# Kernel optimization log

Hardware: AMD Instinct MI355X
Metric: run time of the kernel (lower is better)

Reference implementation:

```python
import jax, jax.numpy as jnp
import numpy as np

D_MODEL = 1024
NUM_HEADS = 16
D_HEAD = D_MODEL // NUM_HEADS
B, T_Q, T_K = 2, 2048, 2048


def setup_inputs() -> dict:
    key = jax.random.key(0)
    ks = jax.random.split(key, 7)
    s = 0.02
    return {
        "query": jax.random.normal(ks[0], (B, T_Q, D_MODEL), jnp.float32),
        "key_value": jax.random.normal(ks[1], (B, T_K, D_MODEL), jnp.float32),
        "mask": jax.random.randint(ks[2], (B, 1, T_Q, T_K), 0, 2, jnp.int32),
        "rel_pos_bias": jax.random.normal(ks[3], (NUM_HEADS, T_Q, T_K), jnp.float32),
        "Wq": jax.random.normal(ks[4], (D_MODEL, D_MODEL), jnp.float32) * s,
        "Wkv": jax.random.normal(ks[5], (D_MODEL, 2 * D_MODEL), jnp.float32) * s,
        "Wo": jax.random.normal(ks[6], (D_MODEL, D_MODEL), jnp.float32) * s,
    }


def reference(query, key_value, mask, rel_pos_bias, Wq, Wkv, Wo):
    Bq, Tq, D = query.shape
    Tk = key_value.shape[1]
    H, Dh = NUM_HEADS, D_HEAD
    q = (query @ Wq).reshape(Bq, Tq, H, Dh)              # [B,Tq,H,Dh]
    kv = (key_value @ Wkv).reshape(Bq, Tk, 2, H, Dh)
    k, v = kv[:, :, 0], kv[:, :, 1]                      # [B,Tk,H,Dh]
    scale = 1.0 / jnp.sqrt(jnp.asarray(Dh, q.dtype))
    scores = jnp.einsum("bqhd,bkhd->bhqk", q, k) * scale  # [B,H,Tq,Tk]
    scores = scores + rel_pos_bias[None]                  # bias broadcast over batch
    scores = jnp.where(mask == 0, -jnp.inf, scores)
    attn = jax.nn.softmax(scores, axis=-1)
    out = jnp.einsum("bhqk,bkhd->bqhd", attn, v).reshape(Bq, Tq, D)
    return out @ Wo
```

## Files before the change

### kernel.cpp

```cpp
#include <hip/hip_runtime.h>

typedef unsigned short u16;
typedef unsigned long long u64;
typedef __attribute__((ext_vector_type(4))) float f32x4;
typedef __attribute__((ext_vector_type(4))) unsigned short u16x4;
typedef __attribute__((ext_vector_type(8))) short short8;

#define GLOAD16(G, L) __builtin_amdgcn_global_load_lds( \
    (const __attribute__((address_space(1))) void*)(G), \
    (__attribute__((address_space(3))) void*)(L), 16, 0, 0)

__device__ __forceinline__ u16 f2bf(float f) {
  union { float f; unsigned u; } c; c.f = f;
  unsigned u = c.u;
  u += 0x7FFFu + ((u >> 16) & 1u);
  return (u16)(u >> 16);
}

__device__ __forceinline__ void store_out(u16* p, float v) { *p = f2bf(v); }
__device__ __forceinline__ void store_out(float* p, float v) { *p = v; }

__global__ void k_cvt(const float* __restrict__ in, u16* __restrict__ out, int n4) {
  int i = blockIdx.x * blockDim.x + threadIdx.x;
  if (i >= n4) return;
  const f32x4 v = *(const f32x4*)(in + (size_t)i * 4);
  u16x4 o;
  o[0] = f2bf(v[0]); o[1] = f2bf(v[1]); o[2] = f2bf(v[2]); o[3] = f2bf(v[3]);
  *(u16x4*)(out + (size_t)i * 4) = o;
}

__global__ void k_tcvt(const float* __restrict__ src, u16* __restrict__ dst,
                       int R, int C, float scale) {
  __shared__ float t[32][33];
  int bx = blockIdx.x * 32;
  int by = blockIdx.y * 32;
  int tx = threadIdx.x, ty = threadIdx.y;
  #pragma unroll
  for (int j = 0; j < 32; j += 8)
    t[ty + j][tx] = src[(size_t)(by + ty + j) * C + bx + tx];
  __syncthreads();
  #pragma unroll
  for (int j = 0; j < 32; j += 8)
    dst[(size_t)(bx + ty + j) * R + by + tx] = f2bf(t[tx][ty + j] * scale);
}

__global__ void k_tv(const u16* __restrict__ kv, u16* __restrict__ vt) {
  __shared__ u16 t[32][34];
  int b = blockIdx.z;
  int tb = blockIdx.x * 32;
  int db = blockIdx.y * 32;
  int tx = threadIdx.x, ty = threadIdx.y;
  #pragma unroll
  for (int j = 0; j < 32; j += 8)
    t[ty + j][tx] = kv[(size_t)(b * 2048 + tb + ty + j) * 2048 + 1024 + db + tx];
  __syncthreads();
  #pragma unroll
  for (int j = 0; j < 32; j += 8)
    vt[(size_t)(b * 1024 + db + ty + j) * 2048 + tb + tx] = t[tx][ty + j];
}

__global__ void k_pm(const int* __restrict__ mask, unsigned* __restrict__ bits, int nw) {
  int w = blockIdx.x * blockDim.x + threadIdx.x;
  if (w >= nw) return;
  const int4* p = (const int4*)(mask + (size_t)w * 32);
  unsigned b = 0;
  #pragma unroll
  for (int j = 0; j < 8; ++j) {
    int4 v = p[j];
    b |= (v.x != 0 ? 1u : 0u) << (j * 4);
    b |= (v.y != 0 ? 1u : 0u) << (j * 4 + 1);
    b |= (v.z != 0 ? 1u : 0u) << (j * 4 + 2);
    b |= (v.w != 0 ? 1u : 0u) << (j * 4 + 3);
  }
  bits[w] = b;
}

template <typename OUT_T>
__global__ __launch_bounds__(256) void k_gemm(
    const u16* __restrict__ A, const u16* __restrict__ Bt,
    OUT_T* __restrict__ C, int M, int N, int K)
{
  __shared__ u16 As[128 * 64];
  __shared__ u16 Bs[128 * 64];
  const int tid = threadIdx.x;
  const int lane = tid & 63;
  const int w = tid >> 6;
  const int wr = w >> 1, wc = w & 1;
  const int l16 = lane & 15, lh = lane >> 4;
  const size_t tm = blockIdx.x, tn = blockIdx.y;

  f32x4 acc[4][4] = {};

  for (int kt = 0; kt < K; kt += 64) {
    #pragma unroll
    for (int i = 0; i < 4; ++i) {
      int flat = i * 256 + tid;
      int row = flat >> 3, cb = flat & 7;
      GLOAD16(A + (tm * 128 + row) * K + kt + ((cb ^ (row & 7)) * 8),
              (char*)As + flat * 16);
    }
    #pragma unroll
    for (int i = 0; i < 4; ++i) {
      int flat = i * 256 + tid;
      int row = flat >> 3, cb = flat & 7;
      GLOAD16(Bt + (tn * 128 + row) * K + kt + ((cb ^ (row & 7)) * 8),
              (char*)Bs + flat * 16);
    }
    __syncthreads();
    #pragma unroll
    for (int kk = 0; kk < 2; ++kk) {
      short8 a[4], b[4];
      #pragma unroll
      for (int mi = 0; mi < 4; ++mi) {
        int row = wr * 64 + mi * 16 + l16;
        a[mi] = *(const short8*)&As[row * 64 + ((kk * 32 + lh * 8) ^ ((row & 7) * 8))];
      }
      #pragma unroll
      for (int ni = 0; ni < 4; ++ni) {
        int row = wc * 64 + ni * 16 + l16;
        b[ni] = *(const short8*)&Bs[row * 64 + ((kk * 32 + lh * 8) ^ ((row & 7) * 8))];
      }
      #pragma unroll
      for (int mi = 0; mi < 4; ++mi)
        #pragma unroll
        for (int ni = 0; ni < 4; ++ni)
          acc[mi][ni] = __builtin_amdgcn_mfma_f32_16x16x32_bf16(a[mi], b[ni], acc[mi][ni], 0, 0, 0);
    }
    __syncthreads();
  }
  #pragma unroll
  for (int mi = 0; mi < 4; ++mi)
    #pragma unroll
    for (int ni = 0; ni < 4; ++ni)
      #pragma unroll
      for (int r = 0; r < 4; ++r) {
        size_t row = tm * 128 + wr * 64 + mi * 16 + lh * 4 + r;
        size_t col = tn * 128 + wc * 64 + ni * 16 + l16;
        store_out(&C[row * N + col], acc[mi][ni][r]);
      }
}

__global__ __launch_bounds__(512, 4) void k_attn(
    const u16* __restrict__ Qp,
    const u16* __restrict__ KVp,
    const u16* __restrict__ Vt,
    const float* __restrict__ bias,
    const unsigned* __restrict__ mbits,
    u16* __restrict__ Ob)
{
  __shared__ u16 Ks[2 * 2 * 64 * 64];
  __shared__ u16 Vs[2 * 2 * 64 * 64];
  __shared__ u16 Ps[8 * 16 * 64];
  const int tid = threadIdx.x;
  const int lane = tid & 63;
  const int w = tid >> 6;
  const int bw = w >> 2;
  const int qs = (w & 3) * 16;
  const int qt = blockIdx.x;
  const int h  = blockIdx.y;
  const int l16 = lane & 15, lh = lane >> 4;

  const int srow = tid >> 3, scb = tid & 7;
  const int scol = (scb ^ (srow & 7)) * 8;
  const u16* ksrc0 = KVp + ((size_t)(          srow)) * 2048 + h * 64 + scol;
  const u16* kstep = KVp;
  const u16* vsrc0 = Vt  + ((size_t)(h * 64 + srow)) * 2048 + scol;

  short8 qf[2];
  {
    size_t row = (size_t)bw * 2048 + qt * 64 + qs + l16;
    qf[0] = *(const short8*)&Qp[row * 1024 + h * 64 + lh * 8];
    qf[1] = *(const short8*)&Qp[row * 1024 + h * 64 + 32 + lh * 8];
  }

  const size_t bias_row = ((size_t)h * 2048 + qt * 64 + qs + lh * 4) * 2048;
  const size_t mrow0 = ((size_t)bw * 2048 + qt * 64 + qs + lh * 4) * 64;

  f32x4 oacc[4] = {};
  float lpart[4] = {0.f, 0.f, 0.f, 0.f};

  {
    GLOAD16(ksrc0 + (size_t)(0 * 2048) * 2048, &Ks[0 * 8192 + 0 * 4096 + tid * 8]);
    GLOAD16(ksrc0 + (size_t)(1 * 2048) * 2048, &Ks[0 * 8192 + 1 * 4096 + tid * 8]);
    GLOAD16(vsrc0 + (size_t)(0 * 1024) * 2048, &Vs[0 * 8192 + 0 * 4096 + tid * 8]);
    GLOAD16(vsrc0 + (size_t)(1 * 1024) * 2048, &Vs[0 * 8192 + 1 * 4096 + tid * 8]);
  }
  f32x4 bias_cur[4];
  u64 mw_cur[4];
  #pragma unroll
  for (int ni = 0; ni < 4; ++ni)
    #pragma unroll
    for (int r = 0; r < 4; ++r)
      bias_cur[ni][r] = bias[bias_row + (size_t)r * 2048 + ni * 16 + l16];
  #pragma unroll
  for (int r = 0; r < 4; ++r)
    mw_cur[r] = *(const u64*)&mbits[mrow0 + (size_t)r * 64];

  asm volatile("s_waitcnt vmcnt(0)" ::: "memory");
  __builtin_amdgcn_s_barrier();

  for (int kt = 0; kt < 32; ++kt) {
    const int cur = kt & 1;

    f32x4 bias_nxt[4];
    u64 mw_nxt[4];
    if (kt + 1 < 32) {
      const int nb = cur ^ 1;
      const size_t kro = (size_t)((kt + 1) * 64) * 2048;
      const size_t vco = (size_t)((kt + 1) * 64);
      GLOAD16(ksrc0 + (size_t)(0 * 2048) * 2048 + kro, &Ks[nb * 8192 + 0 * 4096 + tid * 8]);
      GLOAD16(ksrc0 + (size_t)(1 * 2048) * 2048 + kro, &Ks[nb * 8192 + 1 * 4096 + tid * 8]);
      GLOAD16(vsrc0 + (size_t)(0 * 1024) * 2048 + vco, &Vs[nb * 8192 + 0 * 4096 + tid * 8]);
      GLOAD16(vsrc0 + (size_t)(1 * 1024) * 2048 + vco, &Vs[nb * 8192 + 1 * 4096 + tid * 8]);
      #pragma unroll
      for (int ni = 0; ni < 4; ++ni)
        #pragma unroll
        for (int r = 0; r < 4; ++r)
          bias_nxt[ni][r] = bias[bias_row + (size_t)r * 2048 + (kt + 1) * 64 + ni * 16 + l16];
      #pragma unroll
      for (int r = 0; r < 4; ++r)
        mw_nxt[r] = *(const u64*)&mbits[mrow0 + (size_t)r * 64 + (kt + 1) * 2];
    }

    f32x4 s[4];
    #pragma unroll
    for (int ni = 0; ni < 4; ++ni) s[ni] = bias_cur[ni];
    #pragma unroll
    for (int kk = 0; kk < 2; ++kk) {
      short8 kf[4];
      #pragma unroll
      for (int ni = 0; ni < 4; ++ni) {
        int row = ni * 16 + l16;
        kf[ni] = *(const short8*)&Ks[cur * 8192 + bw * 4096 + row * 64 + ((kk * 32 + lh * 8) ^ ((row & 7) * 8))];
      }
      #pragma unroll
      for (int ni = 0; ni < 4; ++ni)
        s[ni] = __builtin_amdgcn_mfma_f32_16x16x32_bf16(qf[kk], kf[ni], s[ni], 0, 0, 0);
    }

    #pragma unroll
    for (int r = 0; r < 4; ++r) {
      unsigned w0 = (unsigned)mw_cur[r], w1 = (unsigned)(mw_cur[r] >> 32);
      int row16 = lh * 4 + r;
      #pragma unroll
      for (int ni = 0; ni < 4; ++ni) {
        unsigned word = (ni & 2) ? w1 : w0;
        unsigned bit = (word >> ((ni & 1) * 16 + l16)) & 1u;
        float p = bit ? __expf(s[ni][r]) : 0.f;
        lpart[r] += p;
        int col = ni * 16 + l16;
        Ps[w * 1024 + row16 * 64 + (col ^ ((row16 & 7) * 8))] = f2bf(p);
      }
    }

    #pragma unroll
    for (int kk = 0; kk < 2; ++kk) {
      short8 pa, vf[4];
      {
        int row = l16;
        pa = *(const short8*)&Ps[w * 1024 + row * 64 + ((kk * 32 + lh * 8) ^ ((row & 7) * 8))];
      }
      #pragma unroll
      for (int di = 0; di < 4; ++di) {
        int row = di * 16 + l16;
        vf[di] = *(const short8*)&Vs[cur * 8192 + bw * 4096 + row * 64 + ((kk * 32 + lh * 8) ^ ((row & 7) * 8))];
      }
      #pragma unroll
      for (int di = 0; di < 4; ++di)
        oacc[di] = __builtin_amdgcn_mfma_f32_16x16x32_bf16(pa, vf[di], oacc[di], 0, 0, 0);
    }

    #pragma unroll
    for (int ni = 0; ni < 4; ++ni) bias_cur[ni] = bias_nxt[ni];
    #pragma unroll
    for (int r = 0; r < 4; ++r) mw_cur[r] = mw_nxt[r];

    asm volatile("s_waitcnt vmcnt(0)" ::: "memory");
    __builtin_amdgcn_s_barrier();
  }

  #pragma unroll
  for (int r = 0; r < 4; ++r) {
    float sum = lpart[r];
    sum += __shfl_xor(sum, 1);
    sum += __shfl_xor(sum, 2);
    sum += __shfl_xor(sum, 4);
    sum += __shfl_xor(sum, 8);
    float inv = 1.0f / sum;
    size_t row = (size_t)bw * 2048 + qt * 64 + qs + lh * 4 + r;
    #pragma unroll
    for (int di = 0; di < 4; ++di)
      Ob[row * 1024 + h * 64 + di * 16 + l16] = f2bf(oacc[di][r] * inv);
  }
}

extern "C" void kernel_launch(void* const* d_in, const int* in_sizes, int n_in,
                              void* d_out, int out_size, void* d_ws, size_t ws_size,
                              hipStream_t stream) {
  const float* query     = (const float*)d_in[0];
  const float* key_value = (const float*)d_in[1];
  const int*   mask      = (const int*)d_in[2];
  const float* bias      = (const float*)d_in[3];
  const float* Wq        = (const float*)d_in[4];
  const float* Wkv       = (const float*)d_in[5];
  const float* Wo        = (const float*)d_in[6];
  float* out = (float*)d_out;

  char* ws = (char*)d_ws;
  u16* qb   = (u16*)(ws);
  u16* kvb  = (u16*)(ws + 8388608);
  u16* WqT  = (u16*)(ws + 16777216);
  u16* WkvT = (u16*)(ws + 18874368);
  u16* WoT  = (u16*)(ws + 23068672);
  u16* Qp   = (u16*)(ws + 25165824);
  u16* KVp  = (u16*)(ws + 33554432);
  u16* Vt   = (u16*)(ws + 50331648);
  u16* Ob   = (u16*)(ws + 58720256);
  unsigned* mb = (unsigned*)(ws + 67108864);

  dim3 tb(32, 8);
  k_cvt<<<4096, 256, 0, stream>>>(query, qb, 1048576);
  k_cvt<<<4096, 256, 0, stream>>>(key_value, kvb, 1048576);
  k_tcvt<<<dim3(32, 32), tb, 0, stream>>>(Wq,  WqT,  1024, 1024, 0.125f);
  k_tcvt<<<dim3(64, 32), tb, 0, stream>>>(Wkv, WkvT, 1024, 2048, 1.0f);
  k_tcvt<<<dim3(32, 32), tb, 0, stream>>>(Wo,  WoT,  1024, 1024, 1.0f);
  k_pm<<<1024, 256, 0, stream>>>(mask, mb, 262144);
  k_gemm<u16><<<dim3(32, 8),  256, 0, stream>>>(qb,  WqT,  Qp,  4096, 1024, 1024);
  k_gemm<u16><<<dim3(32, 16), 256, 0, stream>>>(kvb, WkvT, KVp, 4096, 2048, 1024);
  k_tv<<<dim3(64, 32, 2), tb, 0, stream>>>(KVp, Vt);
  k_attn<<<dim3(32, 16), 512, 0, stream>>>(Qp, KVp, Vt, bias, mb, Ob);
  k_gemm<float><<<dim3(32, 8), 256, 0, stream>>>(Ob, WoT, out, 4096, 1024, 1024);
}
```

Baseline: 223.0 us.

## Compute transposed score tiles so P stays in registers, dropping LDS round trip

Swaps the MFMA operand order so each lane holds a column of S^T. The exponentiated probabilities can then be packed to bf16 in registers and fed straight into the PV MFMA, with no write to and read back from shared memory. Bias and mask loads become vectorized float4 and single u64 reads, and the V tile gets a new 4-element swizzle. Output stores become packed bf16 pairs, and the row-sum reduction shrinks to two shuffles. The cost is a changed V LDS access pattern with 8-byte reads, which could bring bank conflicts.

```diff
diff --git a/kernel.cpp b/kernel.cpp
--- a/kernel.cpp
+++ b/kernel.cpp
@@ -1,9 +1,11 @@
 #include <hip/hip_runtime.h>
 
 typedef unsigned short u16;
+typedef unsigned int u32;
 typedef unsigned long long u64;
 typedef __attribute__((ext_vector_type(4))) float f32x4;
 typedef __attribute__((ext_vector_type(4))) unsigned short u16x4;
+typedef __attribute__((ext_vector_type(4))) short s16x4;
 typedef __attribute__((ext_vector_type(8))) short short8;
 
 #define GLOAD16(G, L) __builtin_amdgcn_global_load_lds( \
@@ -150,7 +152,6 @@
 {
   __shared__ u16 Ks[2 * 2 * 64 * 64];
   __shared__ u16 Vs[2 * 2 * 64 * 64];
-  __shared__ u16 Ps[8 * 16 * 64];
   const int tid = threadIdx.x;
   const int lane = tid & 63;
   const int w = tid >> 6;
@@ -159,42 +160,35 @@
   const int qt = blockIdx.x;
   const int h  = blockIdx.y;
   const int l16 = lane & 15, lh = lane >> 4;
+  const int q = qt * 64 + qs + l16;
 
   const int srow = tid >> 3, scb = tid & 7;
-  const int scol = (scb ^ (srow & 7)) * 8;
-  const u16* ksrc0 = KVp + ((size_t)(          srow)) * 2048 + h * 64 + scol;
-  const u16* kstep = KVp;
-  const u16* vsrc0 = Vt  + ((size_t)(h * 64 + srow)) * 2048 + scol;
+  const u16* ksrc = KVp + (size_t)srow * 2048 + h * 64 + ((scb ^ (srow & 7)) * 8);
+  const u16* vsrc = Vt + ((size_t)(h * 64 + srow)) * 2048 + (((2 * scb) ^ (srow & 14)) * 4);
 
   short8 qf[2];
   {
-    size_t row = (size_t)bw * 2048 + qt * 64 + qs + l16;
+    size_t row = (size_t)bw * 2048 + q;
     qf[0] = *(const short8*)&Qp[row * 1024 + h * 64 + lh * 8];
     qf[1] = *(const short8*)&Qp[row * 1024 + h * 64 + 32 + lh * 8];
   }
 
-  const size_t bias_row = ((size_t)h * 2048 + qt * 64 + qs + lh * 4) * 2048;
-  const size_t mrow0 = ((size_t)bw * 2048 + qt * 64 + qs + lh * 4) * 64;
+  const float* bsrc = bias + ((size_t)h * 2048 + q) * 2048 + lh * 4;
+  const u64*   msrc = (const u64*)(mbits + ((size_t)bw * 2048 + q) * 64);
 
   f32x4 oacc[4] = {};
-  float lpart[4] = {0.f, 0.f, 0.f, 0.f};
-
-  {
-    GLOAD16(ksrc0 + (size_t)(0 * 2048) * 2048, &Ks[0 * 8192 + 0 * 4096 + tid * 8]);
-    GLOAD16(ksrc0 + (size_t)(1 * 2048) * 2048, &Ks[0 * 8192 + 1 * 4096 + tid * 8]);
-    GLOAD16(vsrc0 + (size_t)(0 * 1024) * 2048, &Vs[0 * 8192 + 0 * 4096 + tid * 8]);
-    GLOAD16(vsrc0 + (size_t)(1 * 1024) * 2048, &Vs[0 * 8192 + 1 * 4096 + tid * 8]);
-  }
+  float lpart = 0.f;
+
+  GLOAD16(ksrc + (size_t)(0 * 2048) * 2048, &Ks[0 * 8192 + 0 * 4096 + tid * 8]);
+  GLOAD16(ksrc + (size_t)(1 * 2048 + 0) * 2048, &Ks[0 * 8192 + 1 * 4096 + tid * 8]);
+  GLOAD16(vsrc + (size_t)(0 * 1024) * 2048, &Vs[0 * 8192 + 0 * 4096 + tid * 8]);
+  GLOAD16(vsrc + (size_t)(1 * 1024) * 2048, &Vs[0 * 8192 + 1 * 4096 + tid * 8]);
+
   f32x4 bias_cur[4];
-  u64 mw_cur[4];
   #pragma unroll
   for (int ni = 0; ni < 4; ++ni)
-    #pragma unroll
-    for (int r = 0; r < 4; ++r)
-      bias_cur[ni][r] = bias[bias_row + (size_t)r * 2048 + ni * 16 + l16];
-  #pragma unroll
-  for (int r = 0; r < 4; ++r)
-    mw_cur[r] = *(const u64*)&mbits[mrow0 + (size_t)r * 64];
+    bias_cur[ni] = *(const f32x4*)(bsrc + 0 * 64 + ni * 16);
+  u64 mw_cur = msrc[0];
 
   asm volatile("s_waitcnt vmcnt(0)" ::: "memory");
   __builtin_amdgcn_s_barrier();
@@ -203,95 +197,98 @@
     const int cur = kt & 1;
 
     f32x4 bias_nxt[4];
-    u64 mw_nxt[4];
+    u64 mw_nxt;
     if (kt + 1 < 32) {
       const int nb = cur ^ 1;
       const size_t kro = (size_t)((kt + 1) * 64) * 2048;
       const size_t vco = (size_t)((kt + 1) * 64);
-      GLOAD16(ksrc0 + (size_t)(0 * 2048) * 2048 + kro, &Ks[nb * 8192 + 0 * 4096 + tid * 8]);
-      GLOAD16(ksrc0 + (size_t)(1 * 2048) * 2048 + kro, &Ks[nb * 8192 + 1 * 4096 + tid * 8]);
-      GLOAD16(vsrc0 + (size_t)(0 * 1024) * 2048 + vco, &Vs[nb * 8192 + 0 * 4096 + tid * 8]);
-      GLOAD16(vsrc0 + (size_t)(1 * 1024) * 2048 + vco, &Vs[nb * 8192 + 1 * 4096 + tid * 8]);
+      GLOAD16(ksrc + (size_t)(0 * 2048) * 2048 + kro, &Ks[nb * 8192 + 0 * 4096 + tid * 8]);
+      GLOAD16(ksrc + (size_t)(1 * 2048) * 2048 + kro, &Ks[nb * 8192 + 1 * 4096 + tid * 8]);
+      GLOAD16(vsrc + (size_t)(0 * 1024) * 2048 + vco, &Vs[nb * 8192 + 0 * 4096 + tid * 8]);
+      GLOAD16(vsrc + (size_t)(1 * 1024) * 2048 + vco, &Vs[nb * 8192 + 1 * 4096 + tid * 8]);
       #pragma unroll
       for (int ni = 0; ni < 4; ++ni)
-        #pragma unroll
-        for (int r = 0; r < 4; ++r)
-          bias_nxt[ni][r] = bias[bias_row + (size_t)r * 2048 + (kt + 1) * 64 + ni * 16 + l16];
-      #pragma unroll
-      for (int r = 0; r < 4; ++r)
-        mw_nxt[r] = *(const u64*)&mbits[mrow0 + (size_t)r * 64 + (kt + 1) * 2];
+        bias_nxt[ni] = *(const f32x4*)(bsrc + (size_t)(kt + 1) * 64 + ni * 16);
+      mw_nxt = msrc[kt + 1];
     }
 
     f32x4 s[4];
     #pragma unroll
     for (int ni = 0; ni < 4; ++ni) s[ni] = bias_cur[ni];
+    const int kbase = cur * 8192 + bw * 4096;
     #pragma unroll
     for (int kk = 0; kk < 2; ++kk) {
       short8 kf[4];
       #pragma unroll
       for (int ni = 0; ni < 4; ++ni) {
         int row = ni * 16 + l16;
-        kf[ni] = *(const short8*)&Ks[cur * 8192 + bw * 4096 + row * 64 + ((kk * 32 + lh * 8) ^ ((row & 7) * 8))];
+        kf[ni] = *(const short8*)&Ks[kbase + row * 64 + ((kk * 32 + lh * 8) ^ ((row & 7) * 8))];
       }
       #pragma unroll
       for (int ni = 0; ni < 4; ++ni)
-        s[ni] = __builtin_amdgcn_mfma_f32_16x16x32_bf16(qf[kk], kf[ni], s[ni], 0, 0, 0);
-    }
-
-    #pragma unroll
-    for (int r = 0; r < 4; ++r) {
-      unsigned w0 = (unsigned)mw_cur[r], w1 = (unsigned)(mw_cur[r] >> 32);
-      int row16 = lh * 4 + r;
+        s[ni] = __builtin_amdgcn_mfma_f32_16x16x32_bf16(kf[ni], qf[kk], s[ni], 0, 0, 0);
+    }
+
+    u32 pb[4][2];
+    {
+      unsigned tlo = (unsigned)(mw_cur) >> (lh * 4);
+      unsigned thi = (unsigned)(mw_cur >> 32) >> (lh * 4);
       #pragma unroll
       for (int ni = 0; ni < 4; ++ni) {
-        unsigned word = (ni & 2) ? w1 : w0;
-        unsigned bit = (word >> ((ni & 1) * 16 + l16)) & 1u;
-        float p = bit ? __expf(s[ni][r]) : 0.f;
-        lpart[r] += p;
-        int col = ni * 16 + l16;
-        Ps[w * 1024 + row16 * 64 + (col ^ ((row16 & 7) * 8))] = f2bf(p);
-      }
-    }
-
+        unsigned tw = (ni < 2) ? tlo : thi;
+        #pragma unroll
+        for (int r = 0; r < 4; ++r) {
+          unsigned bit = (tw >> ((ni & 1) * 16 + r)) & 1u;
+          float pv = bit ? __expf(s[ni][r]) : 0.f;
+          lpart += pv;
+          s[ni][r] = pv;
+        }
+        asm("v_cvt_pk_bf16_f32 %0, %1, %2" : "=v"(pb[ni][0]) : "v"(s[ni][0]), "v"(s[ni][1]));
+        asm("v_cvt_pk_bf16_f32 %0, %1, %2" : "=v"(pb[ni][1]) : "v"(s[ni][2]), "v"(s[ni][3]));
+      }
+    }
+
+    const int vbase = cur * 8192 + bw * 4096;
     #pragma unroll
     for (int kk = 0; kk < 2; ++kk) {
-      short8 pa, vf[4];
-      {
-        int row = l16;
-        pa = *(const short8*)&Ps[w * 1024 + row * 64 + ((kk * 32 + lh * 8) ^ ((row & 7) * 8))];
-      }
+      union { u32 w[4]; short8 v; } pf;
+      pf.w[0] = pb[2 * kk][0];
+      pf.w[1] = pb[2 * kk][1];
+      pf.w[2] = pb[2 * kk + 1][0];
+      pf.w[3] = pb[2 * kk + 1][1];
       #pragma unroll
       for (int di = 0; di < 4; ++di) {
         int row = di * 16 + l16;
-        vf[di] = *(const short8*)&Vs[cur * 8192 + bw * 4096 + row * 64 + ((kk * 32 + lh * 8) ^ ((row & 7) * 8))];
-      }
-      #pragma unroll
-      for (int di = 0; di < 4; ++di)
-        oacc[di] = __builtin_amdgcn_mfma_f32_16x16x32_bf16(pa, vf[di], oacc[di], 0, 0, 0);
+        int sw = row & 14;
+        s16x4 v0 = *(const s16x4*)&Vs[vbase + row * 64 + (((8 * kk + lh) ^ sw) * 4)];
+        s16x4 v1 = *(const s16x4*)&Vs[vbase + row * 64 + (((8 * kk + 4 + lh) ^ sw) * 4)];
+        short8 vf = __builtin_shufflevector(v0, v1, 0, 1, 2, 3, 4, 5, 6, 7);
+        oacc[di] = __builtin_amdgcn_mfma_f32_16x16x32_bf16(vf, pf.v, oacc[di], 0, 0, 0);
+      }
     }
 
     #pragma unroll
     for (int ni = 0; ni < 4; ++ni) bias_cur[ni] = bias_nxt[ni];
-    #pragma unroll
-    for (int r = 0; r < 4; ++r) mw_cur[r] = mw_nxt[r];
+    mw_cur = mw_nxt;
 
     asm volatile("s_waitcnt vmcnt(0)" ::: "memory");
     __builtin_amdgcn_s_barrier();
   }
 
-  #pragma unroll
-  for (int r = 0; r < 4; ++r) {
-    float sum = lpart[r];
-    sum += __shfl_xor(sum, 1);
-    sum += __shfl_xor(sum, 2);
-    sum += __shfl_xor(sum, 4);
-    sum += __shfl_xor(sum, 8);
-    float inv = 1.0f / sum;
-    size_t row = (size_t)bw * 2048 + qt * 64 + qs + lh * 4 + r;
-    #pragma unroll
-    for (int di = 0; di < 4; ++di)
-      Ob[row * 1024 + h * 64 + di * 16 + l16] = f2bf(oacc[di][r] * inv);
-  }
+  lpart += __shfl_xor(lpart, 16);
+  lpart += __shfl_xor(lpart, 32);
+  float inv = 1.0f / lpart;
+  size_t orow = (size_t)bw * 2048 + q;
+  #pragma unroll
+  for (int di = 0; di < 4; ++di)
+    #pragma unroll
+    for (int rp = 0; rp < 2; ++rp) {
+      float v0 = oacc[di][2 * rp] * inv;
+      float v1 = oacc[di][2 * rp + 1] * inv;
+      u32 pk;
+      asm("v_cvt_pk_bf16_f32 %0, %1, %2" : "=v"(pk) : "v"(v0), "v"(v1));
+      *(u32*)&Ob[orow * 1024 + h * 64 + di * 16 + lh * 4 + rp * 2] = pk;
+    }
 }
 
 extern "C" void kernel_launch(void* const* d_in, const int* in_sizes, int n_in,
```

After: 250.5 us. 1.12x slower.
